# Kernel tuning notes

Hardware: AMD Instinct MI355X
Metric: run time of the kernel (lower is better)

The kernel has to match this reference:

```python
import jax, jax.numpy as jnp
import numpy as np
import math

D_MODEL = 2048
N_HEADS = 16
D_K = D_MODEL // N_HEADS  # 128
B = 2
L = 2048


def _rope_cos_sin(seq_len, d_k, dtype):
    inv_freq = 1.0 / (10000.0 ** (jnp.arange(0, d_k, 2, dtype=jnp.float32) / d_k))
    t = jnp.arange(seq_len, dtype=jnp.float32)
    freqs = jnp.outer(t, inv_freq)  # [L, d_k//2]
    return jnp.cos(freqs).astype(dtype), jnp.sin(freqs).astype(dtype)


def _apply_rope(x, cos, sin):
    # x: [B, H, L, d_k]; cos/sin: [L, d_k//2] broadcast over B,H
    half = x.shape[-1] // 2
    x1, x2 = x[..., :half], x[..., half:]
    c = cos[None, None, :, :]
    s = sin[None, None, :, :]
    return jnp.concatenate([x1 * c - x2 * s, x1 * s + x2 * c], axis=-1)


def setup_inputs() -> dict:
    key = jax.random.key(0)
    ks = jax.random.split(key, 8)
    scale = 1.0 / math.sqrt(D_MODEL)
    query = jax.random.normal(ks[0], (B, L, D_MODEL), dtype=jnp.float32)
    k_in = jax.random.normal(ks[1], (B, L, D_MODEL), dtype=jnp.float32)
    v_in = jax.random.normal(ks[2], (B, L, D_MODEL), dtype=jnp.float32)
    w_q = jax.random.normal(ks[3], (D_MODEL, D_MODEL), dtype=jnp.float32) * scale
    w_k = jax.random.normal(ks[4], (D_MODEL, D_MODEL), dtype=jnp.float32) * scale
    w_v = jax.random.normal(ks[5], (D_MODEL, D_MODEL), dtype=jnp.float32) * scale
    w_o = jax.random.normal(ks[6], (D_MODEL, D_MODEL), dtype=jnp.float32) * scale
    mask = jnp.tril(jnp.ones((L, L), dtype=bool))[None, None, :, :]
    return {"query": query, "key": k_in, "value": v_in, "mask": mask,
            "w_q": w_q, "w_k": w_k, "w_v": w_v, "w_o": w_o}


def reference(query, key, value, mask, w_q, w_k, w_v, w_o):
    Bq, Lq, D = query.shape
    Lk = key.shape[1]
    # Linear (no bias): y = x @ W.T ; split heads -> [B, H, L, d_k]
    def proj(x, w, length):
        y = jnp.einsum('bld,ed->ble', x, w)
        return y.reshape(x.shape[0], length, N_HEADS, D_K).transpose(0, 2, 1, 3)
    Q = proj(query, w_q, Lq)
    K = proj(key, w_k, Lk)
    V = proj(value, w_v, Lk)
    cos_q, sin_q = _rope_cos_sin(Lq, D_K, query.dtype)
    cos_k, sin_k = _rope_cos_sin(Lk, D_K, key.dtype)
    Q = _apply_rope(Q, cos_q, sin_q)
    K = _apply_rope(K, cos_k, sin_k)
    scores = jnp.einsum('bhqd,bhkd->bhqk', Q, K) / math.sqrt(D_K)
    neg = jnp.finfo(scores.dtype).min
    scores = jnp.where(mask, scores, neg)
    attn = jax.nn.softmax(scores, axis=-1)
    out = jnp.einsum('bhqk,bhkd->bhqd', attn, V)
    out = out.transpose(0, 2, 1, 3).reshape(Bq, Lq, D)
    return jnp.einsum('bld,ed->ble', out, w_o)
```

## Files before the change

### kernel.cpp

```cpp
#include <hip/hip_runtime.h>
#include <stdint.h>

#define L_SEQ 2048
#define DMODEL 2048
#define NHEADS 16
#define DK 128
#define BATCH 2
#define MROWS (BATCH*L_SEQ)

typedef float f32x4 __attribute__((ext_vector_type(4)));
typedef short s16x8 __attribute__((ext_vector_type(8)));
typedef unsigned short u16;
typedef unsigned int u32;

__device__ __forceinline__ u16 f2bf(float f){
  u32 u = __builtin_bit_cast(u32, f);
  u += 0x7fffu + ((u >> 16) & 1u);
  return (u16)(u >> 16);
}
__device__ __forceinline__ float bf2f(u16 h){
  u32 u = ((u32)h) << 16;
  return __builtin_bit_cast(float, u);
}
__device__ __forceinline__ void gload_lds16(const void* g, void* l){
  __builtin_amdgcn_global_load_lds((const __attribute__((address_space(1))) void*)g,
                                   (__attribute__((address_space(3))) void*)l, 16, 0, 0);
}

__global__ void k_cvt_all(const float* __restrict__ s0, const float* __restrict__ s1,
                          const float* __restrict__ s2, const float* __restrict__ s3,
                          const float* __restrict__ s4, const float* __restrict__ s5,
                          const float* __restrict__ s6,
                          u16* __restrict__ d0, u16* __restrict__ d1, u16* __restrict__ d2,
                          u16* __restrict__ d3, u16* __restrict__ d4, u16* __restrict__ d5,
                          u16* __restrict__ d6,
                          float* __restrict__ ct, float* __restrict__ st){
  const int XC = MROWS*DMODEL/8;
  const int WC = DMODEL*DMODEL/8;
  const int total = 3*XC + 4*WC;
  const int TBL = L_SEQ*64;
  int stride = gridDim.x * blockDim.x;
  for (int i = blockIdx.x*blockDim.x + threadIdx.x; i < total + TBL; i += stride){
    if (i >= total){
      int idx = i - total;
      int lq = idx >> 6, d = idx & 63;
      float e = (float)d * (1.0f/64.0f);
      float inv = 1.0f / powf(10000.0f, e);
      float fr = (float)lq * inv;
      ct[idx] = cosf(fr);
      st[idx] = sinf(fr);
      continue;
    }
    const float* s; u16* d; int j;
    if (i < XC)        { s=s0; d=d0; j=i; }
    else if (i < 2*XC) { s=s1; d=d1; j=i-XC; }
    else if (i < 3*XC) { s=s2; d=d2; j=i-2*XC; }
    else {
      int k2 = i - 3*XC; int wi = k2 / WC; j = k2 - wi*WC;
      s = wi==0?s3 : wi==1?s4 : wi==2?s5 : s6;
      d = wi==0?d3 : wi==1?d4 : wi==2?d5 : d6;
    }
    const f32x4* sp = (const f32x4*)s + (size_t)j*2;
    f32x4 a = sp[0], b = sp[1];
    s16x8 o;
    o[0]=(short)f2bf(a[0]); o[1]=(short)f2bf(a[1]); o[2]=(short)f2bf(a[2]); o[3]=(short)f2bf(a[3]);
    o[4]=(short)f2bf(b[0]); o[5]=(short)f2bf(b[1]); o[6]=(short)f2bf(b[2]); o[7]=(short)f2bf(b[3]);
    ((s16x8*)d)[j] = o;
  }
}

__global__ void k_ropeK(u16* __restrict__ xk,
                        const float* __restrict__ ct, const float* __restrict__ st){
  int t = blockIdx.x*blockDim.x + threadIdx.x;
  int i8  = (t & 7) * 8;
  int h   = (t >> 3) & 15;
  int row = t >> 7;
  int l   = row & (L_SEQ-1);
  u16* p = xk + (size_t)row*DMODEL + h*DK;
  s16x8 a  = *(s16x8*)(p + i8);
  s16x8 bq = *(s16x8*)(p + 64 + i8);
  const float* cp = ct + l*64 + i8;
  const float* sp = st + l*64 + i8;
  f32x4 c0 = *(const f32x4*)cp, c1 = *(const f32x4*)(cp+4);
  f32x4 s0 = *(const f32x4*)sp, s1 = *(const f32x4*)(sp+4);
  float cc[8] = {c0[0],c0[1],c0[2],c0[3],c1[0],c1[1],c1[2],c1[3]};
  float ss[8] = {s0[0],s0[1],s0[2],s0[3],s1[0],s1[1],s1[2],s1[3]};
  s16x8 y1, y2;
  #pragma unroll
  for (int e=0;e<8;e++){
    float x1 = bf2f((u16)a[e]), x2 = bf2f((u16)bq[e]);
    y1[e] = (short)f2bf(x1*cc[e] - x2*ss[e]);
    y2[e] = (short)f2bf(x1*ss[e] + x2*cc[e]);
  }
  *(s16x8*)(p + i8)      = y1;
  *(s16x8*)(p + 64 + i8) = y2;
}

__global__ __launch_bounds__(256)
void k_gemm3(const u16* __restrict__ A0, const u16* __restrict__ A1, const u16* __restrict__ A2,
             const u16* __restrict__ B0, const u16* __restrict__ B1, const u16* __restrict__ B2,
             u16* __restrict__ C0, u16* __restrict__ C1, u16* __restrict__ C2){
  __shared__ u16 As[128*64];
  __shared__ u16 Bs[128*64];
  const int z = blockIdx.z;
  const u16* __restrict__ A  = z==0?A0 : z==1?A1 : A2;
  const u16* __restrict__ Bw = z==0?B0 : z==1?B1 : B2;
  u16* __restrict__ Cb       = z==0?C0 : z==1?C1 : C2;
  const int tid = threadIdx.x, w = tid>>6, l = tid&63;
  const int lg = l>>4, lr = l&15;
  const int lin = (int)blockIdx.y*16 + (int)blockIdx.x;
  const int lin2 = (lin&7)*64 + (lin>>3);
  const int bm = (lin2>>4)*128, bn = (lin2&15)*128;
  const int K = DMODEL, N = DMODEL;
  f32x4 acc[4][4];
  #pragma unroll
  for (int i=0;i<4;i++)
    #pragma unroll
    for (int j=0;j<4;j++) acc[i][j] = (f32x4){0.f,0.f,0.f,0.f};

  const int chunkbase = w*64 + l;
  const int wm = (w>>1)*64, wn = (w&1)*64;

  for (int k0 = 0; k0 < K; k0 += 64){
    __syncthreads();
    #pragma unroll
    for (int i=0;i<4;i++){
      int chunk = i*256 + chunkbase;
      int row = chunk >> 3;
      int cbs = ((chunk&7)<<4) ^ ((row&7)<<4);
      const u16* ga = A  + (size_t)(bm+row)*K + k0 + (cbs>>1);
      const u16* gb = Bw + (size_t)(bn+row)*K + k0 + (cbs>>1);
      gload_lds16(ga, (void*)&As[(i*256 + w*64)*8]);
      gload_lds16(gb, (void*)&Bs[(i*256 + w*64)*8]);
    }
    __syncthreads();
    #pragma unroll
    for (int kc=0; kc<2; kc++){
      s16x8 af[4], bfr[4];
      #pragma unroll
      for (int mi=0; mi<4; mi++){
        int row = wm + mi*16 + lr;
        int off = row*128 + ((kc*64 + lg*16) ^ ((row&7)<<4));
        af[mi] = *(const s16x8*)((const char*)As + off);
      }
      #pragma unroll
      for (int ni=0; ni<4; ni++){
        int row = wn + ni*16 + lr;
        int off = row*128 + ((kc*64 + lg*16) ^ ((row&7)<<4));
        bfr[ni] = *(const s16x8*)((const char*)Bs + off);
      }
      #pragma unroll
      for (int mi=0; mi<4; mi++)
        #pragma unroll
        for (int ni=0; ni<4; ni++)
          acc[mi][ni] = __builtin_amdgcn_mfma_f32_16x16x32_bf16(af[mi], bfr[ni], acc[mi][ni], 0,0,0);
    }
  }
  #pragma unroll
  for (int mi=0; mi<4; mi++)
    #pragma unroll
    for (int ni=0; ni<4; ni++)
      #pragma unroll
      for (int r=0; r<4; r++){
        int row = bm + wm + mi*16 + (lg<<2) + r;
        int col = bn + wn + ni*16 + lr;
        Cb[(size_t)row*N + col] = f2bf(acc[mi][ni][r]);
      }
}

__global__ __launch_bounds__(256)
void k_gemm(const u16* __restrict__ A, const u16* __restrict__ Bw,
            float* __restrict__ Cf){
  __shared__ u16 As[128*64];
  __shared__ u16 Bs[128*64];
  const int tid = threadIdx.x, w = tid>>6, l = tid&63;
  const int lg = l>>4, lr = l&15;
  const int lin = (int)blockIdx.y*16 + (int)blockIdx.x;
  const int lin2 = (lin&7)*64 + (lin>>3);
  const int bm = (lin2>>4)*128, bn = (lin2&15)*128;
  const int K = DMODEL, N = DMODEL;
  f32x4 acc[4][4];
  #pragma unroll
  for (int i=0;i<4;i++)
    #pragma unroll
    for (int j=0;j<4;j++) acc[i][j] = (f32x4){0.f,0.f,0.f,0.f};

  const int chunkbase = w*64 + l;
  const int wm = (w>>1)*64, wn = (w&1)*64;

  for (int k0 = 0; k0 < K; k0 += 64){
    __syncthreads();
    #pragma unroll
    for (int i=0;i<4;i++){
      int chunk = i*256 + chunkbase;
      int row = chunk >> 3;
      int cbs = ((chunk&7)<<4) ^ ((row&7)<<4);
      const u16* ga = A  + (size_t)(bm+row)*K + k0 + (cbs>>1);
      const u16* gb = Bw + (size_t)(bn+row)*K + k0 + (cbs>>1);
      gload_lds16(ga, (void*)&As[(i*256 + w*64)*8]);
      gload_lds16(gb, (void*)&Bs[(i*256 + w*64)*8]);
    }
    __syncthreads();
    #pragma unroll
    for (int kc=0; kc<2; kc++){
      s16x8 af[4], bfr[4];
      #pragma unroll
      for (int mi=0; mi<4; mi++){
        int row = wm + mi*16 + lr;
        int off = row*128 + ((kc*64 + lg*16) ^ ((row&7)<<4));
        af[mi] = *(const s16x8*)((const char*)As + off);
      }
      #pragma unroll
      for (int ni=0; ni<4; ni++){
        int row = wn + ni*16 + lr;
        int off = row*128 + ((kc*64 + lg*16) ^ ((row&7)<<4));
        bfr[ni] = *(const s16x8*)((const char*)Bs + off);
      }
      #pragma unroll
      for (int mi=0; mi<4; mi++)
        #pragma unroll
        for (int ni=0; ni<4; ni++)
          acc[mi][ni] = __builtin_amdgcn_mfma_f32_16x16x32_bf16(af[mi], bfr[ni], acc[mi][ni], 0,0,0);
    }
  }
  #pragma unroll
  for (int mi=0; mi<4; mi++)
    #pragma unroll
    for (int ni=0; ni<4; ni++)
      #pragma unroll
      for (int r=0; r<4; r++){
        int row = bm + wm + mi*16 + (lg<<2) + r;
        int col = bn + wn + ni*16 + lr;
        Cf[(size_t)row*N + col] = acc[mi][ni][r];
      }
}

__global__ __launch_bounds__(256)
void k_attn(const u16* __restrict__ Qp, const u16* __restrict__ Kp,
            const u16* __restrict__ Vp, u16* __restrict__ AO,
            const float* __restrict__ ct, const float* __restrict__ st){
  __shared__ u16 Ks[2][64*128];
  __shared__ u16 Vs[128*64];
  __shared__ u16 Ps[4][16*72];
  const int tid = threadIdx.x, w = tid>>6, l = tid&63;
  const int lg = l>>4, lr = l&15;
  const int lin = (int)blockIdx.y * (int)gridDim.x + (int)blockIdx.x;
  const int xcd = lin & 7, s8 = lin >> 3;
  const int bh  = xcd*4 + (s8 >> 4);
  const int qtp = s8 & 15;
  const int b = bh>>4, h = bh&15;
  const size_t kvbase = (size_t)(b*L_SEQ)*DMODEL + h*DK;
  const float scale = 0.08838834764831845f;

  u32 vv[2][8];
  s16x8 ones;
  #pragma unroll
  for (int e=0;e<8;e++) ones[e] = (short)0x3F80;

  auto issueK = [&](int j, int buf){
    #pragma unroll
    for (int i=0;i<4;i++){
      int chunk = i*256 + w*64 + l;
      int row = chunk >> 4;
      int cb = ((chunk&15)<<4) ^ ((row&7)<<4);
      const u16* src = Kp + kvbase + (size_t)(j*64 + row)*DMODEL + (cb>>1);
      gload_lds16(src, (void*)&Ks[buf][(i*256 + w*64)*8]);
    }
  };
  auto issueV = [&](int j){
    #pragma unroll
    for (int it=0; it<2; it++){
      int task = it*256 + tid;
      int dp = task & 63, kb = task >> 6;
      const u16* vsrc = Vp + kvbase + (size_t)(j*64 + kb*8)*DMODEL + dp*2;
      #pragma unroll
      for (int e=0;e<8;e++) vv[it][e] = *(const u32*)(vsrc + (size_t)e*DMODEL);
    }
  };
  auto writeV = [&](){
    #pragma unroll
    for (int it=0; it<2; it++){
      int task = it*256 + tid;
      int dp = task & 63, kb = task >> 6;
      int d0 = dp*2;
      s16x8 lo, hi;
      #pragma unroll
      for (int e=0;e<8;e++){ lo[e] = (short)(vv[it][e] & 0xffffu); hi[e] = (short)(vv[it][e] >> 16); }
      int g = ((d0>>1)&7)<<4;
      *(s16x8*)((char*)&Vs[0] + d0*128     + ((kb*16) ^ g)) = lo;
      *(s16x8*)((char*)&Vs[0] + (d0+1)*128 + ((kb*16) ^ g)) = hi;
    }
  };

  for (int half=0; half<2; half++){
    const int qt = half==0 ? qtp : 31-qtp;
    if (half) __syncthreads();

    s16x8 qf[4];
    {
      const int lq = qt*64 + w*16 + lr;
      const u16* qptr = Qp + (size_t)(b*L_SEQ + lq)*DMODEL + h*DK + lg*8;
      #pragma unroll
      for (int kc=0; kc<4; kc++) qf[kc] = *(const s16x8*)(qptr + kc*32);
      #pragma unroll
      for (int kc=0; kc<2; kc++){
        const float* cp = ct + lq*64 + kc*32 + lg*8;
        const float* sp = st + lq*64 + kc*32 + lg*8;
        f32x4 c0 = *(const f32x4*)cp, c1 = *(const f32x4*)(cp+4);
        f32x4 s0 = *(const f32x4*)sp, s1 = *(const f32x4*)(sp+4);
        float cc[8] = {c0[0],c0[1],c0[2],c0[3],c1[0],c1[1],c1[2],c1[3]};
        float ss[8] = {s0[0],s0[1],s0[2],s0[3],s1[0],s1[1],s1[2],s1[3]};
        #pragma unroll
        for (int e=0;e<8;e++){
          float x1 = bf2f((u16)qf[kc][e]), x2 = bf2f((u16)qf[kc+2][e]);
          qf[kc][e]   = (short)f2bf(x1*cc[e] - x2*ss[e]);
          qf[kc+2][e] = (short)f2bf(x1*ss[e] + x2*cc[e]);
        }
      }
    }
    f32x4 o[9];
    #pragma unroll
    for (int dt=0; dt<9; dt++) o[dt] = (f32x4){0.f,0.f,0.f,0.f};
    float mrow[4] = {-1e30f,-1e30f,-1e30f,-1e30f};

    issueK(0, 0);
    issueV(0);

    for (int j=0; j<=qt; j++){
      const int cur = j & 1;
      asm volatile("s_waitcnt vmcnt(16)" ::: "memory");
      __builtin_amdgcn_sched_barrier(0);
      __builtin_amdgcn_s_barrier();
      __builtin_amdgcn_sched_barrier(0);
      if (j < qt) issueK(j+1, cur^1);

      f32x4 st4[4];
      __builtin_amdgcn_s_setprio(1);
      #pragma unroll
      for (int ni=0; ni<4; ni++){
        f32x4 a = (f32x4){0.f,0.f,0.f,0.f};
        #pragma unroll
        for (int kc=0; kc<4; kc++){
          int row = ni*16 + lr;
          int off = row*256 + ((kc*64 + lg*16) ^ ((row&7)<<4));
          s16x8 kf = *(const s16x8*)((const char*)&Ks[cur][0] + off);
          a = __builtin_amdgcn_mfma_f32_16x16x32_bf16(qf[kc], kf, a, 0,0,0);
        }
        st4[ni] = a;
      }
      __builtin_amdgcn_s_setprio(0);

      float sv[4][4];
      float lanemax = -1e30f;
      const bool diag = (j == qt);
      #pragma unroll
      for (int r=0;r<4;r++){
        #pragma unroll
        for (int ni=0;ni<4;ni++){
          float x = st4[ni][r]*scale;
          if (diag){
            int kg = ni*16 + lr;
            int qg = w*16 + lg*4 + r;
            if (kg > qg) x = -1e30f;
          }
          sv[ni][r] = x;
          lanemax = fmaxf(lanemax, x);
        }
      }
      float mmin = fminf(fminf(mrow[0],mrow[1]), fminf(mrow[2],mrow[3]));
      if (!__all(lanemax <= mmin + 8.0f)){
        #pragma unroll
        for (int r=0;r<4;r++){
          float tm = fmaxf(fmaxf(sv[0][r],sv[1][r]), fmaxf(sv[2][r],sv[3][r]));
          #pragma unroll
          for (int msk=1; msk<16; msk<<=1) tm = fmaxf(tm, __shfl_xor(tm, msk, 64));
          float mn = fmaxf(mrow[r], tm);
          float al = __expf(mrow[r]-mn);
          mrow[r] = mn;
          #pragma unroll
          for (int dt=0;dt<9;dt++) o[dt][r] *= al;
        }
      }
      #pragma unroll
      for (int r=0;r<4;r++){
        #pragma unroll
        for (int ni=0;ni<4;ni++){
          float p = __expf(sv[ni][r]-mrow[r]);
          Ps[w][(lg*4 + r)*72 + ni*16 + lr] = f2bf(p);
        }
      }
      s16x8 pa[2];
      #pragma unroll
      for (int kc=0;kc<2;kc++) pa[kc] = *(const s16x8*)(&Ps[w][lr*72 + kc*32 + lg*8]);

      if (j < qt){ asm volatile("s_waitcnt vmcnt(4)" ::: "memory"); }
      else       { asm volatile("s_waitcnt vmcnt(0)" ::: "memory"); }
      __builtin_amdgcn_sched_barrier(0);
      writeV();
      if (j < qt) issueV(j+1);
      asm volatile("s_waitcnt lgkmcnt(0)" ::: "memory");
      __builtin_amdgcn_sched_barrier(0);
      __builtin_amdgcn_s_barrier();
      __builtin_amdgcn_sched_barrier(0);

      __builtin_amdgcn_s_setprio(1);
      #pragma unroll
      for (int dt=0;dt<8;dt++){
        #pragma unroll
        for (int kc=0;kc<2;kc++){
          int d = dt*16 + lr;
          int off = d*128 + ((kc*64 + lg*16) ^ (((d>>1)&7)<<4));
          s16x8 vf = *(const s16x8*)((const char*)&Vs[0] + off);
          o[dt] = __builtin_amdgcn_mfma_f32_16x16x32_bf16(pa[kc], vf, o[dt], 0,0,0);
        }
      }
      o[8] = __builtin_amdgcn_mfma_f32_16x16x32_bf16(pa[0], ones, o[8], 0,0,0);
      o[8] = __builtin_amdgcn_mfma_f32_16x16x32_bf16(pa[1], ones, o[8], 0,0,0);
      __builtin_amdgcn_s_setprio(0);
    }

    #pragma unroll
    for (int r=0;r<4;r++){
      float inv = 1.0f / o[8][r];
      size_t rowg = (size_t)(b*L_SEQ + qt*64 + w*16 + lg*4 + r);
      #pragma unroll
      for (int dt=0;dt<8;dt++)
        AO[rowg*DMODEL + h*DK + dt*16 + lr] = f2bf(o[dt][r]*inv);
    }
  }
}

extern "C" void kernel_launch(void* const* d_in, const int* in_sizes, int n_in,
                              void* d_out, int out_size, void* d_ws, size_t ws_size,
                              hipStream_t stream){
  const float* q  = (const float*)d_in[0];
  const float* k  = (const float*)d_in[1];
  const float* v  = (const float*)d_in[2];
  const float* wq = (const float*)d_in[4];
  const float* wk = (const float*)d_in[5];
  const float* wv = (const float*)d_in[6];
  const float* wo = (const float*)d_in[7];
  (void)in_sizes; (void)n_in; (void)out_size; (void)ws_size;

  const size_t MD = (size_t)MROWS*DMODEL;
  const size_t DD = (size_t)DMODEL*DMODEL;
  char* ws = (char*)d_ws;
  size_t off = 0;
  auto alloc = [&](size_t bytes)->void*{ void* p = ws + off; off += (bytes + 255) & ~(size_t)255; return p; };
  u16* Xq = (u16*)alloc(MD*2);
  u16* Xk = (u16*)alloc(MD*2);
  u16* Xv = (u16*)alloc(MD*2);
  u16* Wq = (u16*)alloc(DD*2);
  u16* Wk = (u16*)alloc(DD*2);
  u16* Wv = (u16*)alloc(DD*2);
  u16* Wo = (u16*)alloc(DD*2);
  u16* Qp = (u16*)alloc(MD*2);
  u16* Kp = (u16*)alloc(MD*2);
  u16* Vp = (u16*)alloc(MD*2);
  float* ct = (float*)alloc((size_t)L_SEQ*64*4);
  float* st = (float*)alloc((size_t)L_SEQ*64*4);
  u16* AO = Xq;

  k_cvt_all<<<2048,256,0,stream>>>(q, k, v, wq, wk, wv, wo,
                                   Xq, Xk, Xv, Wq, Wk, Wv, Wo, ct, st);

  k_gemm3<<<dim3(16,32,3),256,0,stream>>>(Xq, Xk, Xv, Wq, Wk, Wv, Qp, Kp, Vp);
  k_ropeK<<<2048,256,0,stream>>>(Kp, ct, st);
  k_attn<<<dim3(16,32),256,0,stream>>>(Qp, Kp, Vp, AO, ct, st);
  k_gemm<<<dim3(16,32),256,0,stream>>>(AO, Wo, (float*)d_out);
}
```

Before: 275.5 us.

## Double-buffer QKV projection GEMM with 128x256 tiles and 512-thread blocks

Reworks the fused QKV projection GEMM to use 128x256 block tiles with 8 waves and double-buffered LDS. The next K-stage is prefetched while the current one feeds interleaved MFMA groups, with s_setprio and sched_barrier steering the schedule. This targets the load/compute serialization of the old single-buffered loop and raises B-tile reuse. In exchange it uses more LDS per block (96KB) and halves the grid, which may lower occupancy and tail balance.

New measurement: 278.4 us. About the same (+1.1%).

```diff
diff --git a/kernel.cpp b/kernel.cpp
--- a/kernel.cpp
+++ b/kernel.cpp
@@ -96,21 +96,22 @@
   *(s16x8*)(p + 64 + i8) = y2;
 }
 
-__global__ __launch_bounds__(256)
-void k_gemm3(const u16* __restrict__ A0, const u16* __restrict__ A1, const u16* __restrict__ A2,
-             const u16* __restrict__ B0, const u16* __restrict__ B1, const u16* __restrict__ B2,
+__global__ __launch_bounds__(512)
+void k_gemm3(const u16* __restrict__ A0p, const u16* __restrict__ A1p, const u16* __restrict__ A2p,
+             const u16* __restrict__ B0p, const u16* __restrict__ B1p, const u16* __restrict__ B2p,
              u16* __restrict__ C0, u16* __restrict__ C1, u16* __restrict__ C2){
-  __shared__ u16 As[128*64];
-  __shared__ u16 Bs[128*64];
+  __shared__ u16 As[2][128*64];
+  __shared__ u16 Bs[2][256*64];
   const int z = blockIdx.z;
-  const u16* __restrict__ A  = z==0?A0 : z==1?A1 : A2;
-  const u16* __restrict__ Bw = z==0?B0 : z==1?B1 : B2;
+  const u16* __restrict__ A  = z==0?A0p : z==1?A1p : A2p;
+  const u16* __restrict__ Bw = z==0?B0p : z==1?B1p : B2p;
   u16* __restrict__ Cb       = z==0?C0 : z==1?C1 : C2;
   const int tid = threadIdx.x, w = tid>>6, l = tid&63;
   const int lg = l>>4, lr = l&15;
-  const int lin = (int)blockIdx.y*16 + (int)blockIdx.x;
-  const int lin2 = (lin&7)*64 + (lin>>3);
-  const int bm = (lin2>>4)*128, bn = (lin2&15)*128;
+  const int wr = w>>2, wc = w&3;
+  const int lin = (int)blockIdx.y*8 + (int)blockIdx.x;
+  const int lin2 = (lin&7)*32 + (lin>>3);
+  const int bm = (lin2>>3)*128, bn = (lin2&7)*256;
   const int K = DMODEL, N = DMODEL;
   f32x4 acc[4][4];
   #pragma unroll
@@ -118,43 +119,89 @@
     #pragma unroll
     for (int j=0;j<4;j++) acc[i][j] = (f32x4){0.f,0.f,0.f,0.f};
 
-  const int chunkbase = w*64 + l;
-  const int wm = (w>>1)*64, wn = (w&1)*64;
-
-  for (int k0 = 0; k0 < K; k0 += 64){
-    __syncthreads();
-    #pragma unroll
-    for (int i=0;i<4;i++){
-      int chunk = i*256 + chunkbase;
+  auto stage = [&](int s, int buf){
+    const int k0 = s*64;
+    #pragma unroll
+    for (int i=0;i<2;i++){
+      int chunk = i*512 + tid;
       int row = chunk >> 3;
       int cbs = ((chunk&7)<<4) ^ ((row&7)<<4);
-      const u16* ga = A  + (size_t)(bm+row)*K + k0 + (cbs>>1);
-      const u16* gb = Bw + (size_t)(bn+row)*K + k0 + (cbs>>1);
-      gload_lds16(ga, (void*)&As[(i*256 + w*64)*8]);
-      gload_lds16(gb, (void*)&Bs[(i*256 + w*64)*8]);
-    }
-    __syncthreads();
-    #pragma unroll
-    for (int kc=0; kc<2; kc++){
-      s16x8 af[4], bfr[4];
-      #pragma unroll
-      for (int mi=0; mi<4; mi++){
-        int row = wm + mi*16 + lr;
-        int off = row*128 + ((kc*64 + lg*16) ^ ((row&7)<<4));
-        af[mi] = *(const s16x8*)((const char*)As + off);
-      }
-      #pragma unroll
-      for (int ni=0; ni<4; ni++){
-        int row = wn + ni*16 + lr;
-        int off = row*128 + ((kc*64 + lg*16) ^ ((row&7)<<4));
-        bfr[ni] = *(const s16x8*)((const char*)Bs + off);
-      }
-      #pragma unroll
-      for (int mi=0; mi<4; mi++)
-        #pragma unroll
-        for (int ni=0; ni<4; ni++)
-          acc[mi][ni] = __builtin_amdgcn_mfma_f32_16x16x32_bf16(af[mi], bfr[ni], acc[mi][ni], 0,0,0);
-    }
+      gload_lds16(A + (size_t)(bm+row)*K + k0 + (cbs>>1), (void*)&As[buf][chunk*8]);
+    }
+    #pragma unroll
+    for (int i=0;i<4;i++){
+      int chunk = i*512 + tid;
+      int row = chunk >> 3;
+      int cbs = ((chunk&7)<<4) ^ ((row&7)<<4);
+      gload_lds16(Bw + (size_t)(bn+row)*K + k0 + (cbs>>1), (void*)&Bs[buf][chunk*8]);
+    }
+  };
+  auto ard = [&](int buf, int h, int kc, int j)->s16x8{
+    int row = wr*64 + h*32 + j*16 + lr;
+    int off = row*128 + ((kc*64 + lg*16) ^ ((row&7)<<4));
+    return *(const s16x8*)((const char*)&As[buf][0] + off);
+  };
+  auto brd = [&](int buf, int kc, int ni)->s16x8{
+    int row = wc*64 + ni*16 + lr;
+    int off = row*128 + ((kc*64 + lg*16) ^ ((row&7)<<4));
+    return *(const s16x8*)((const char*)&Bs[buf][0] + off);
+  };
+
+  stage(0, 0);
+  const int nt = K/64;
+  for (int s=0; s<nt; s++){
+    const int cur = s&1;
+    asm volatile("s_waitcnt vmcnt(0)" ::: "memory");
+    __builtin_amdgcn_sched_barrier(0);
+    __builtin_amdgcn_s_barrier();
+    __builtin_amdgcn_sched_barrier(0);
+
+    s16x8 Bk0[4], Ah0[2], Ah1[2];
+    #pragma unroll
+    for (int ni=0;ni<4;ni++) Bk0[ni] = brd(cur,0,ni);
+    Ah0[0] = ard(cur,0,0,0); Ah0[1] = ard(cur,0,0,1);
+    Ah1[0] = ard(cur,1,0,0); Ah1[1] = ard(cur,1,0,1);
+    if (s+1 < nt) stage(s+1, cur^1);
+    __builtin_amdgcn_sched_barrier(0);
+    __builtin_amdgcn_s_setprio(1);
+    #pragma unroll
+    for (int ni=0;ni<4;ni++){
+      acc[0][ni] = __builtin_amdgcn_mfma_f32_16x16x32_bf16(Ah0[0], Bk0[ni], acc[0][ni], 0,0,0);
+      acc[1][ni] = __builtin_amdgcn_mfma_f32_16x16x32_bf16(Ah0[1], Bk0[ni], acc[1][ni], 0,0,0);
+    }
+    __builtin_amdgcn_s_setprio(0);
+    s16x8 Bk1[4], Ah2[2];
+    #pragma unroll
+    for (int ni=0;ni<4;ni++) Bk1[ni] = brd(cur,1,ni);
+    Ah2[0] = ard(cur,0,1,0); Ah2[1] = ard(cur,0,1,1);
+    __builtin_amdgcn_sched_barrier(0);
+    __builtin_amdgcn_s_setprio(1);
+    #pragma unroll
+    for (int ni=0;ni<4;ni++){
+      acc[2][ni] = __builtin_amdgcn_mfma_f32_16x16x32_bf16(Ah1[0], Bk0[ni], acc[2][ni], 0,0,0);
+      acc[3][ni] = __builtin_amdgcn_mfma_f32_16x16x32_bf16(Ah1[1], Bk0[ni], acc[3][ni], 0,0,0);
+    }
+    __builtin_amdgcn_s_setprio(0);
+    s16x8 Ah3[2];
+    Ah3[0] = ard(cur,1,1,0); Ah3[1] = ard(cur,1,1,1);
+    __builtin_amdgcn_sched_barrier(0);
+    __builtin_amdgcn_s_setprio(1);
+    #pragma unroll
+    for (int ni=0;ni<4;ni++){
+      acc[0][ni] = __builtin_amdgcn_mfma_f32_16x16x32_bf16(Ah2[0], Bk1[ni], acc[0][ni], 0,0,0);
+      acc[1][ni] = __builtin_amdgcn_mfma_f32_16x16x32_bf16(Ah2[1], Bk1[ni], acc[1][ni], 0,0,0);
+    }
+    __builtin_amdgcn_s_setprio(0);
+    __builtin_amdgcn_sched_barrier(0);
+    __builtin_amdgcn_s_setprio(1);
+    #pragma unroll
+    for (int ni=0;ni<4;ni++){
+      acc[2][ni] = __builtin_amdgcn_mfma_f32_16x16x32_bf16(Ah3[0], Bk1[ni], acc[2][ni], 0,0,0);
+      acc[3][ni] = __builtin_amdgcn_mfma_f32_16x16x32_bf16(Ah3[1], Bk1[ni], acc[3][ni], 0,0,0);
+    }
+    __builtin_amdgcn_s_setprio(0);
+    __builtin_amdgcn_sched_barrier(0);
+    __builtin_amdgcn_s_barrier();
   }
   #pragma unroll
   for (int mi=0; mi<4; mi++)
@@ -162,8 +209,8 @@
     for (int ni=0; ni<4; ni++)
       #pragma unroll
       for (int r=0; r<4; r++){
-        int row = bm + wm + mi*16 + (lg<<2) + r;
-        int col = bn + wn + ni*16 + lr;
+        int row = bm + wr*64 + mi*16 + (lg<<2) + r;
+        int col = bn + wc*64 + ni*16 + lr;
         Cb[(size_t)row*N + col] = f2bf(acc[mi][ni][r]);
       }
 }
@@ -464,7 +511,7 @@
   k_cvt_all<<<2048,256,0,stream>>>(q, k, v, wq, wk, wv, wo,
                                    Xq, Xk, Xv, Wq, Wk, Wv, Wo, ct, st);
 
-  k_gemm3<<<dim3(16,32,3),256,0,stream>>>(Xq, Xk, Xv, Wq, Wk, Wv, Qp, Kp, Vp);
+  k_gemm3<<<dim3(8,32,3),512,0,stream>>>(Xq, Xk, Xv, Wq, Wk, Wv, Qp, Kp, Vp);
   k_ropeK<<<2048,256,0,stream>>>(Kp, ct, st);
   k_attn<<<dim3(16,32),256,0,stream>>>(Qp, Kp, Vp, AO, ct, st);
   k_gemm<<<dim3(16,32),256,0,stream>>>(AO, Wo, (float*)d_out);
```
